# Performance work log

Measured on AMD Instinct MI355X. Metric: run time of the kernel, lower is better.

The kernel has to match this reference:

```python
import jax, jax.numpy as jnp
import numpy as np

IMAGE_SIZE = 128
FACES_PER_PIXEL = 4
BLUR_RADIUS = 0.01
EPS = 1e-8


def setup_inputs() -> dict:
    key = jax.random.key(0)
    k1, k2, k3 = jax.random.split(key, 3)
    B, V, F = 2, 2000, 800
    # verts are already projected to screen/NDC space: x,y in [-1,1], z > 0 (depth)
    xy = jax.random.uniform(k1, (B, V, 2), minval=-1.0, maxval=1.0)
    z = jax.random.uniform(k2, (B, V, 1), minval=0.5, maxval=2.5)
    verts = jnp.concatenate([xy, z], axis=-1).astype(jnp.float32)
    faces = jax.random.randint(k3, (F, 3), 0, V)
    return {"verts": verts, "faces": faces}


def _edge(a, b, p):
    # signed parallelogram area of (a -> b -> p), using xy components only
    return (p[..., 0] - a[..., 0]) * (b[..., 1] - a[..., 1]) - (
        p[..., 1] - a[..., 1]) * (b[..., 0] - a[..., 0])


def _seg_dist2(p, a, b):
    # squared distance from point p to segment [a, b] in 2D
    ab = b - a
    pa = p - a
    t = jnp.clip(jnp.sum(pa * ab, -1) / (jnp.sum(ab * ab, -1) + EPS), 0.0, 1.0)
    d = pa - t[..., None] * ab
    return jnp.sum(d * d, -1)


def _rasterize(verts, faces):
    H = W = IMAGE_SIZE
    K = FACES_PER_PIXEL
    B = verts.shape[0]
    fv = verts[:, faces]                      # [B,F,3,3] gather face vertices
    v0, v1, v2 = fv[:, :, 0], fv[:, :, 1], fv[:, :, 2]
    a0 = v0[:, None, :, :2]                   # [B,1,F,2]
    a1 = v1[:, None, :, :2]
    a2 = v2[:, None, :, :2]
    z0 = v0[:, None, :, 2]                    # [B,1,F]
    z1 = v1[:, None, :, 2]
    z2 = v2[:, None, :, 2]
    # pixel centers in NDC, pytorch3d convention: index 0 -> +1, last -> -1
    xs = 1.0 - 2.0 * (jnp.arange(W, dtype=verts.dtype) + 0.5) / W
    ys = 1.0 - 2.0 * (jnp.arange(H, dtype=verts.dtype) + 0.5) / H
    yy, xx = jnp.meshgrid(ys, xs, indexing="ij")
    p = jnp.stack([xx, yy], -1).reshape(1, -1, 1, 2)   # [1,P,1,2], P=H*W

    area = _edge(a0, a1, a2)                  # [B,1,F] signed face area*2
    w0 = _edge(a1, a2, p)                     # [B,P,F]
    w1 = _edge(a2, a0, p)
    w2 = _edge(a0, a1, p)
    denom = jnp.where(jnp.abs(area) > EPS, area,
                      jnp.where(area >= 0, EPS, -EPS))
    b0, b1, b2 = w0 / denom, w1 / denom, w2 / denom
    zpix = b0 * z0 + b1 * z1 + b2 * z2        # [B,P,F] interpolated depth

    inside = (b0 >= 0) & (b1 >= 0) & (b2 >= 0)
    dmin = jnp.minimum(_seg_dist2(p, a0, a1),
                       jnp.minimum(_seg_dist2(p, a1, a2),
                                   _seg_dist2(p, a2, a0)))
    dsign = jnp.where(inside, -dmin, dmin)    # signed squared edge distance

    valid = (inside | (dmin < BLUR_RADIUS)) & (zpix > EPS) & (
        jnp.abs(area) > EPS)
    zcand = jnp.where(valid, zpix, jnp.inf)
    _, idx = jax.lax.top_k(-zcand, K)         # K nearest faces per pixel

    take = lambda x: jnp.take_along_axis(x, idx, axis=-1)
    sel_valid = take(valid)
    pix_to_face = jnp.where(sel_valid, idx, -1)
    zbuf = jnp.where(sel_valid, take(zpix), -1.0)
    bary = jnp.stack([b0, b1, b2], -1)        # [B,P,F,3]
    bsel = jnp.take_along_axis(bary, idx[..., None], axis=2)  # [B,P,K,3]
    bsel = jnp.where(sel_valid[..., None], bsel, -1.0)
    dsel = jnp.where(sel_valid, take(dsign), -1.0)

    return (pix_to_face.reshape(B, H, W, K),
            zbuf.reshape(B, H, W, K),
            bsel.reshape(B, H, W, K, 3),
            dsel.reshape(B, H, W, K))


def reference(verts, faces):
    # Fragments: (pix_to_face, zbuf, bary_coords, dists)
    return _rasterize(verts, faces)
```

## Files before the change

### kernel.cpp

```cpp
#include <hip/hip_runtime.h>

#define IMG   128
#define KF    4
#define NF    800
#define NV    2000
#define NB    2
#define EPSF  1e-8f
#define BLURF 0.01f
#define CULL_D2 0.0103f
#define HEXT    0.0547f

typedef unsigned long long u64;
#define INVK ((((u64)0x7f800000u) << 32) | 0xffffffffu)

#pragma clang fp contract(off)

__device__ __forceinline__ float rcp2(float d) {
    float y = __builtin_amdgcn_rcpf(d);
    float e = __builtin_fmaf(-d, y, 1.0f);
    y = __builtin_fmaf(y, e, y);
    e = __builtin_fmaf(-d, y, 1.0f);
    y = __builtin_fmaf(y, e, y);
    return y;
}
__device__ __forceinline__ float fdivr(float n, float d, float y) {
    float q0 = n * y;
    float r  = __builtin_fmaf(-d, q0, n);
    return __builtin_fmaf(r, y, q0);
}

__device__ __forceinline__ float seg_d2(float pax, float pay, float abx, float aby) {
#pragma clang fp contract(off)
    float dd = (abx * abx + aby * aby) + EPSF;
    float t  = (pax * abx + pay * aby) / dd;
    t = fminf(fmaxf(t, 0.0f), 1.0f);
    float dx = pax - t * abx;
    float dy = pay - t * aby;
    return dx * dx + dy * dy;
}

__device__ __forceinline__ float seg_d2y(float pax, float pay, float abx, float aby, float y) {
#pragma clang fp contract(off)
    float dd = (abx * abx + aby * aby) + EPSF;
    float n  = pax * abx + pay * aby;
    float t  = fdivr(n, dd, y);
    t = fminf(fmaxf(t, 0.0f), 1.0f);
    float dx = pax - t * abx;
    float dy = pay - t * aby;
    return dx * dx + dy * dy;
}

__device__ __forceinline__ void ins4(u64& s0, u64& s1, u64& s2, u64& s3, u64 k) {
    bool c0 = k < s0, c1 = k < s1, c2 = k < s2, c3 = k < s3;
    s3 = c2 ? s2 : (c3 ? k : s3);
    s2 = c1 ? s1 : (c2 ? k : s2);
    s1 = c0 ? s0 : (c1 ? k : s1);
    s0 = c0 ? k  : s0;
}

__global__ __launch_bounds__(256) void raster_p1(
    const float* __restrict__ verts,
    const int*   __restrict__ faces,
    u64* __restrict__ ws,
    int sh)
{
#pragma clang fp contract(off)
    extern __shared__ __align__(16) float sFD[];
    __shared__ u64 sK[2 * 4 * 64];
    __shared__ int sTot;

    const int S     = 1 << sh;
    const int chunk = NF >> sh;

    const int tid   = threadIdx.x;
    const int blk   = blockIdx.x;
    const int tile  = blk >> sh;
    const int slice = blk & (S - 1);
    const int b     = tile >> 8;
    const int trow  = (tile & 255) >> 4;
    const int tcol  = tile & 15;
    const float* vb = verts + b * NV * 3;
    const int fbase = slice * chunk;

    if (tid == 0) sTot = 0;

    const float txmax = 1.0f - (2.0f * ((float)(tcol * 8)     + 0.5f)) / 128.0f;
    const float txmin = 1.0f - (2.0f * ((float)(tcol * 8 + 7) + 0.5f)) / 128.0f;
    const float tymax = 1.0f - (2.0f * ((float)(trow * 8)     + 0.5f)) / 128.0f;
    const float tymin = 1.0f - (2.0f * ((float)(trow * 8 + 7) + 0.5f)) / 128.0f;
    const float cx = 0.5f * (txmin + txmax);
    const float cy = 0.5f * (tymin + tymax);

    __syncthreads();

    for (int j = tid; j < chunk; j += 256) {
        int f = fbase + j;
        int i0 = faces[3 * f + 0], i1 = faces[3 * f + 1], i2 = faces[3 * f + 2];
        float a0x = vb[3 * i0], a0y = vb[3 * i0 + 1], z0 = vb[3 * i0 + 2];
        float a1x = vb[3 * i1], a1y = vb[3 * i1 + 1], z1 = vb[3 * i1 + 2];
        float a2x = vb[3 * i2], a2y = vb[3 * i2 + 1], z2 = vb[3 * i2 + 2];
        float area = (a2x - a0x) * (a1y - a0y) - (a2y - a0y) * (a1x - a0x);
        bool surv = fabsf(area) > EPSF;
        float bxmin = fminf(a0x, fminf(a1x, a2x)) - 0.101f;
        float bxmax = fmaxf(a0x, fmaxf(a1x, a2x)) + 0.101f;
        float bymin = fminf(a0y, fminf(a1y, a2y)) - 0.101f;
        float bymax = fmaxf(a0y, fmaxf(a1y, a2y)) + 0.101f;
        surv &= !(bxmin > txmax || bxmax < txmin || bymin > tymax || bymax < tymin);
        float s = (area >= 0.0f) ? 1.0f : -1.0f;
        float e0x = a2x - a1x, e0y = a2y - a1y;
        float e1x = a0x - a2x, e1y = a0y - a2y;
        float e2x = a1x - a0x, e2y = a1y - a0y;
        float w0 = s * ((cx - a1x) * e0y - (cy - a1y) * e0x) + HEXT * (fabsf(e0x) + fabsf(e0y));
        float w1 = s * ((cx - a2x) * e1y - (cy - a2y) * e1x) + HEXT * (fabsf(e1x) + fabsf(e1y));
        float w2 = s * ((cx - a0x) * e2y - (cy - a0y) * e2x) + HEXT * (fabsf(e2x) + fabsf(e2y));
        float l0 = e0x * e0x + e0y * e0y;
        float l1 = e1x * e1x + e1y * e1y;
        float l2 = e2x * e2x + e2y * e2y;
        surv &= !((w0 < 0.0f) & (w0 * w0 > CULL_D2 * l0));
        surv &= !((w1 < 0.0f) & (w1 * w1 > CULL_D2 * l1));
        surv &= !((w2 < 0.0f) & (w2 * w2 > CULL_D2 * l2));
        if (surv) {
            int pos = atomicAdd(&sTot, 1);
            float yd  = rcp2(area);
            float ylA = rcp2(l2 + EPSF);
            float ylB = rcp2(l0 + EPSF);
            float ylC = rcp2(l1 + EPSF);
            float4* fd = (float4*)&sFD[pos * 16];
            fd[0] = make_float4(a0x, a0y, a1x, a1y);
            fd[1] = make_float4(a2x, a2y, z0, z1);
            fd[2] = make_float4(z2, area, yd, __int_as_float(f));
            fd[3] = make_float4(ylA, ylB, ylC, 0.0f);
        }
    }
    __syncthreads();
    const int total = sTot;

    const int wave = tid >> 6;
    const int lane = tid & 63;
    const int pr = lane >> 3, pc = lane & 7;
    const int row = trow * 8 + pr, col = tcol * 8 + pc;
    const float px = 1.0f - (2.0f * ((float)col + 0.5f)) / 128.0f;
    const float py = 1.0f - (2.0f * ((float)row + 0.5f)) / 128.0f;

    u64 s0 = INVK, s1 = INVK, s2 = INVK, s3 = INVK;
    for (int j = wave; j < total; j += 4) {
        const float4* fd = (const float4*)&sFD[j * 16];
        float4 r0 = fd[0];
        float4 r1 = fd[1];
        float4 r2 = fd[2];
        float4 r3 = fd[3];
        float a0x = r0.x, a0y = r0.y, a1x = r0.z, a1y = r0.w;
        float a2x = r1.x, a2y = r1.y, z0 = r1.z, z1 = r1.w;
        float z2 = r2.x, denom = r2.y, yd = r2.z;
        unsigned fi = __float_as_uint(r2.w);
        float ylA = r3.x, ylB = r3.y, ylC = r3.z;

        float e0x = a2x - a1x, e0y = a2y - a1y;
        float e1x = a0x - a2x, e1y = a0y - a2y;
        float e2x = a1x - a0x, e2y = a1y - a0y;
        float p0x = px - a0x, p0y = py - a0y;
        float p1x = px - a1x, p1y = py - a1y;
        float p2x = px - a2x, p2y = py - a2y;
        float w0 = p1x * e0y - p1y * e0x;
        float w1 = p2x * e1y - p2y * e1x;
        float w2 = p0x * e2y - p0y * e2x;
        float b0 = fdivr(w0, denom, yd);
        float b1 = fdivr(w1, denom, yd);
        float b2 = fdivr(w2, denom, yd);
        float zpix = (b0 * z0 + b1 * z1) + b2 * z2;
        bool inside = fminf(b0, fminf(b1, b2)) >= 0.0f;
        bool valid;
        if (__all(inside)) {
            valid = (zpix > EPSF);
        } else {
            float dA = seg_d2y(p0x, p0y, e2x, e2y, ylA);
            float dB = seg_d2y(p1x, p1y, e0x, e0y, ylB);
            float dC = seg_d2y(p2x, p2y, e1x, e1y, ylC);
            float dmin = fminf(dA, fminf(dB, dC));
            valid = (inside | (dmin < BLURF)) & (zpix > EPSF);
        }
        u64 key = valid ? ((((u64)__float_as_uint(zpix)) << 32) | (u64)fi) : INVK;
        if (__any(key < s3)) ins4(s0, s1, s2, s3, key);
    }

    if (wave >= 2) {
        int r = wave - 2;
        sK[(r * 4 + 0) * 64 + lane] = s0;
        sK[(r * 4 + 1) * 64 + lane] = s1;
        sK[(r * 4 + 2) * 64 + lane] = s2;
        sK[(r * 4 + 3) * 64 + lane] = s3;
    }
    __syncthreads();
    if (wave < 2) {
        ins4(s0, s1, s2, s3, sK[(wave * 4 + 0) * 64 + lane]);
        ins4(s0, s1, s2, s3, sK[(wave * 4 + 1) * 64 + lane]);
        ins4(s0, s1, s2, s3, sK[(wave * 4 + 2) * 64 + lane]);
        ins4(s0, s1, s2, s3, sK[(wave * 4 + 3) * 64 + lane]);
    }
    __syncthreads();
    if (wave == 1) {
        sK[0 * 64 + lane] = s0;
        sK[1 * 64 + lane] = s1;
        sK[2 * 64 + lane] = s2;
        sK[3 * 64 + lane] = s3;
    }
    __syncthreads();
    if (wave == 0) {
        ins4(s0, s1, s2, s3, sK[0 * 64 + lane]);
        ins4(s0, s1, s2, s3, sK[1 * 64 + lane]);
        ins4(s0, s1, s2, s3, sK[2 * 64 + lane]);
        ins4(s0, s1, s2, s3, sK[3 * 64 + lane]);
        u64* wrow = ws + (size_t)blk * 256;
        wrow[0 * 64 + lane] = s0;
        wrow[1 * 64 + lane] = s1;
        wrow[2 * 64 + lane] = s2;
        wrow[3 * 64 + lane] = s3;
    }
}

__global__ __launch_bounds__(256) void raster_p2(
    const float* __restrict__ verts,
    const int*   __restrict__ faces,
    const u64* __restrict__ ws,
    int sh,
    float* __restrict__ out0, float* __restrict__ out1,
    float* __restrict__ out2, float* __restrict__ out3)
{
#pragma clang fp contract(off)
    __shared__ u64 sK[4 * 64];
    const int S    = 1 << sh;
    const int tid  = threadIdx.x;
    const int tile = blockIdx.x;
    const int b    = tile >> 8;
    const int trow = (tile & 255) >> 4;
    const int tcol = tile & 15;
    const float* vb = verts + b * NV * 3;

    if (tid < 64) {
        u64 s0 = INVK, s1 = INVK, s2 = INVK, s3 = INVK;
        const u64* base = ws + (size_t)tile * S * 256;
        for (int s = 0; s < S; ++s) {
            ins4(s0, s1, s2, s3, base[s * 256 + 0 * 64 + tid]);
            ins4(s0, s1, s2, s3, base[s * 256 + 1 * 64 + tid]);
            ins4(s0, s1, s2, s3, base[s * 256 + 2 * 64 + tid]);
            ins4(s0, s1, s2, s3, base[s * 256 + 3 * 64 + tid]);
        }
        sK[0 * 64 + tid] = s0;
        sK[1 * 64 + tid] = s1;
        sK[2 * 64 + tid] = s2;
        sK[3 * 64 + tid] = s3;
    }
    __syncthreads();

    int pix = tid >> 2, k = tid & 3;
    u64 key = sK[k * 64 + pix];
    int prow = pix >> 3, pcol = pix & 7;
    int grow = trow * 8 + prow, gcol = tcol * 8 + pcol;
    int p = (b * IMG + grow) * IMG + gcol;
    float qx = 1.0f - (2.0f * ((float)gcol + 0.5f)) / 128.0f;
    float qy = 1.0f - (2.0f * ((float)grow + 0.5f)) / 128.0f;
    float o0 = -1.0f, o1 = -1.0f, ob0 = -1.0f, ob1 = -1.0f, ob2 = -1.0f, o3 = -1.0f;
    if ((unsigned)(key >> 32) != 0x7f800000u) {
        int fi = (int)(unsigned)(key & 0xffffffffu);
        int i0 = faces[3 * fi + 0], i1 = faces[3 * fi + 1], i2 = faces[3 * fi + 2];
        float a0x = vb[3 * i0], a0y = vb[3 * i0 + 1], z0 = vb[3 * i0 + 2];
        float a1x = vb[3 * i1], a1y = vb[3 * i1 + 1], z1 = vb[3 * i1 + 2];
        float a2x = vb[3 * i2], a2y = vb[3 * i2 + 1], z2 = vb[3 * i2 + 2];
        float area = (a2x - a0x) * (a1y - a0y) - (a2y - a0y) * (a1x - a0x);
        float aab  = fabsf(area);
        float denom = (aab > EPSF) ? area : (area >= 0.0f ? EPSF : -EPSF);
        float e0x = a2x - a1x, e0y = a2y - a1y;
        float e1x = a0x - a2x, e1y = a0y - a2y;
        float e2x = a1x - a0x, e2y = a1y - a0y;
        float p0x = qx - a0x, p0y = qy - a0y;
        float p1x = qx - a1x, p1y = qy - a1y;
        float p2x = qx - a2x, p2y = qy - a2y;
        float w0 = p1x * e0y - p1y * e0x;
        float w1 = p2x * e1y - p2y * e1x;
        float w2 = p0x * e2y - p0y * e2x;
        float b0 = w0 / denom, b1 = w1 / denom, b2 = w2 / denom;
        float zpix = (b0 * z0 + b1 * z1) + b2 * z2;
        bool inside = (b0 >= 0.0f) & (b1 >= 0.0f) & (b2 >= 0.0f);
        float dA = seg_d2(p0x, p0y, e2x, e2y);
        float dB = seg_d2(p1x, p1y, e0x, e0y);
        float dC = seg_d2(p2x, p2y, e1x, e1y);
        float dmin = fminf(dA, fminf(dB, dC));
        o0 = (float)fi;
        o1 = zpix;
        ob0 = b0; ob1 = b1; ob2 = b2;
        o3 = inside ? -dmin : dmin;
    }
    int o = p * KF + k;
    out0[o] = o0;
    out1[o] = o1;
    out2[o * 3 + 0] = ob0;
    out2[o * 3 + 1] = ob1;
    out2[o * 3 + 2] = ob2;
    out3[o] = o3;
}

extern "C" void kernel_launch(void* const* d_in, const int* in_sizes, int n_in,
                              void* d_out, int out_size, void* d_ws, size_t ws_size,
                              hipStream_t stream) {
    const float* verts = (const float*)d_in[0];
    const int*   faces = (const int*)d_in[1];
    float* out = (float*)d_out;
    const int n0 = NB * IMG * IMG * KF;

    const size_t per_slice = 512ull * 256 * sizeof(u64);
    int sh;
    if      (ws_size >= 4 * per_slice) sh = 2;
    else if (ws_size >= 2 * per_slice) sh = 1;
    else                               sh = 0;
    const int S = 1 << sh;
    const int chunk = NF >> sh;
    const size_t dyn = (size_t)chunk * 16 * sizeof(float);

    raster_p1<<<dim3(512 * S), dim3(256), dyn, stream>>>(verts, faces, (u64*)d_ws, sh);
    raster_p2<<<dim3(512), dim3(256), 0, stream>>>(verts, faces, (const u64*)d_ws, sh,
        out,
        out + n0,
        out + 2 * n0,
        out + 5 * n0);
}
```

Before: 81.62 us.

## Bin surviving faces by conservative min depth and early-exit per-pixel loop

Each surviving face gets a conservative minimum depth over the tile corners and is bucketed into one of eight depth bins. Faces are compacted into shared memory in bin order using a prefix sum. The per-pixel loop walks bins front to back and stops once every lane's fourth-best key lies below the next bin's lower bound, skipping far faces. This adds an extra barrier, a serial prefix step and per-face corner depth evaluation. It depends on the slack constants and the sliver-area fallback being conservative enough to keep results exact.

```diff
diff --git a/kernel.cpp b/kernel.cpp
--- a/kernel.cpp
+++ b/kernel.cpp
@@ -9,6 +9,8 @@
 #define BLURF 0.01f
 #define CULL_D2 0.0103f
 #define HEXT    0.0547f
+#define AREA_SLIVER 0.01f
+#define ZSLACK  0.05f
 
 typedef unsigned long long u64;
 #define INVK ((((u64)0x7f800000u) << 32) | 0xffffffffu)
@@ -58,6 +60,45 @@
     s0 = c0 ? k  : s0;
 }
 
+__device__ __forceinline__ u64 eval_rec(const float4* fd, float px, float py) {
+#pragma clang fp contract(off)
+    float4 r0 = fd[0];
+    float4 r1 = fd[1];
+    float4 r2 = fd[2];
+    float4 r3 = fd[3];
+    float a0x = r0.x, a0y = r0.y, a1x = r0.z, a1y = r0.w;
+    float a2x = r1.x, a2y = r1.y, z0 = r1.z, z1 = r1.w;
+    float z2 = r2.x, denom = r2.y, yd = r2.z;
+    unsigned fi = __float_as_uint(r2.w);
+    float ylA = r3.x, ylB = r3.y, ylC = r3.z;
+
+    float e0x = a2x - a1x, e0y = a2y - a1y;
+    float e1x = a0x - a2x, e1y = a0y - a2y;
+    float e2x = a1x - a0x, e2y = a1y - a0y;
+    float p0x = px - a0x, p0y = py - a0y;
+    float p1x = px - a1x, p1y = py - a1y;
+    float p2x = px - a2x, p2y = py - a2y;
+    float w0 = p1x * e0y - p1y * e0x;
+    float w1 = p2x * e1y - p2y * e1x;
+    float w2 = p0x * e2y - p0y * e2x;
+    float b0 = fdivr(w0, denom, yd);
+    float b1 = fdivr(w1, denom, yd);
+    float b2 = fdivr(w2, denom, yd);
+    float zpix = (b0 * z0 + b1 * z1) + b2 * z2;
+    bool inside = fminf(b0, fminf(b1, b2)) >= 0.0f;
+    bool valid;
+    if (__all(inside)) {
+        valid = (zpix > EPSF);
+    } else {
+        float dA = seg_d2y(p0x, p0y, e2x, e2y, ylA);
+        float dB = seg_d2y(p1x, p1y, e0x, e0y, ylB);
+        float dC = seg_d2y(p2x, p2y, e1x, e1y, ylC);
+        float dmin = fminf(dA, fminf(dB, dC));
+        valid = (inside | (dmin < BLURF)) & (zpix > EPSF);
+    }
+    return valid ? ((((u64)__float_as_uint(zpix)) << 32) | (u64)fi) : INVK;
+}
+
 __global__ __launch_bounds__(256) void raster_p1(
     const float* __restrict__ verts,
     const int*   __restrict__ faces,
@@ -68,6 +109,9 @@
     extern __shared__ __align__(16) float sFD[];
     __shared__ u64 sK[2 * 4 * 64];
     __shared__ int sTot;
+    __shared__ int binCnt[8];
+    __shared__ int binCur[8];
+    __shared__ int binStartS[9];
 
     const int S     = 1 << sh;
     const int chunk = NF >> sh;
@@ -83,6 +127,7 @@
     const int fbase = slice * chunk;
 
     if (tid == 0) sTot = 0;
+    if (tid < 8) binCnt[tid] = 0;
 
     const float txmax = 1.0f - (2.0f * ((float)(tcol * 8)     + 0.5f)) / 128.0f;
     const float txmin = 1.0f - (2.0f * ((float)(tcol * 8 + 7) + 0.5f)) / 128.0f;
@@ -93,47 +138,126 @@
 
     __syncthreads();
 
-    for (int j = tid; j < chunk; j += 256) {
-        int f = fbase + j;
-        int i0 = faces[3 * f + 0], i1 = faces[3 * f + 1], i2 = faces[3 * f + 2];
-        float a0x = vb[3 * i0], a0y = vb[3 * i0 + 1], z0 = vb[3 * i0 + 2];
-        float a1x = vb[3 * i1], a1y = vb[3 * i1 + 1], z1 = vb[3 * i1 + 2];
-        float a2x = vb[3 * i2], a2y = vb[3 * i2 + 1], z2 = vb[3 * i2 + 2];
-        float area = (a2x - a0x) * (a1y - a0y) - (a2y - a0y) * (a1x - a0x);
-        bool surv = fabsf(area) > EPSF;
-        float bxmin = fminf(a0x, fminf(a1x, a2x)) - 0.101f;
-        float bxmax = fmaxf(a0x, fmaxf(a1x, a2x)) + 0.101f;
-        float bymin = fminf(a0y, fminf(a1y, a2y)) - 0.101f;
-        float bymax = fmaxf(a0y, fmaxf(a1y, a2y)) + 0.101f;
-        surv &= !(bxmin > txmax || bxmax < txmin || bymin > tymax || bymax < tymin);
-        float s = (area >= 0.0f) ? 1.0f : -1.0f;
-        float e0x = a2x - a1x, e0y = a2y - a1y;
-        float e1x = a0x - a2x, e1y = a0y - a2y;
-        float e2x = a1x - a0x, e2y = a1y - a0y;
-        float w0 = s * ((cx - a1x) * e0y - (cy - a1y) * e0x) + HEXT * (fabsf(e0x) + fabsf(e0y));
-        float w1 = s * ((cx - a2x) * e1y - (cy - a2y) * e1x) + HEXT * (fabsf(e1x) + fabsf(e1y));
-        float w2 = s * ((cx - a0x) * e2y - (cy - a0y) * e2x) + HEXT * (fabsf(e2x) + fabsf(e2y));
-        float l0 = e0x * e0x + e0y * e0y;
-        float l1 = e1x * e1x + e1y * e1y;
-        float l2 = e2x * e2x + e2y * e2y;
-        surv &= !((w0 < 0.0f) & (w0 * w0 > CULL_D2 * l0));
-        surv &= !((w1 < 0.0f) & (w1 * w1 > CULL_D2 * l1));
-        surv &= !((w2 < 0.0f) & (w2 * w2 > CULL_D2 * l2));
+    if (chunk <= 256) {
+        bool surv = false;
+        int bin = 0;
+        float a0x=0, a0y=0, a1x=0, a1y=0, a2x=0, a2y=0, z0=0, z1=0, z2=0;
+        float area=0, yd=0, ylA=0, ylB=0, ylC=0;
+        int f = fbase + tid;
+        if (tid < chunk) {
+            int i0 = faces[3 * f + 0], i1 = faces[3 * f + 1], i2 = faces[3 * f + 2];
+            a0x = vb[3 * i0]; a0y = vb[3 * i0 + 1]; z0 = vb[3 * i0 + 2];
+            a1x = vb[3 * i1]; a1y = vb[3 * i1 + 1]; z1 = vb[3 * i1 + 2];
+            a2x = vb[3 * i2]; a2y = vb[3 * i2 + 1]; z2 = vb[3 * i2 + 2];
+            area = (a2x - a0x) * (a1y - a0y) - (a2y - a0y) * (a1x - a0x);
+            surv = fabsf(area) > EPSF;
+            float bxmin = fminf(a0x, fminf(a1x, a2x)) - 0.101f;
+            float bxmax = fmaxf(a0x, fmaxf(a1x, a2x)) + 0.101f;
+            float bymin = fminf(a0y, fminf(a1y, a2y)) - 0.101f;
+            float bymax = fmaxf(a0y, fmaxf(a1y, a2y)) + 0.101f;
+            surv &= !(bxmin > txmax || bxmax < txmin || bymin > tymax || bymax < tymin);
+            float s = (area >= 0.0f) ? 1.0f : -1.0f;
+            float e0x = a2x - a1x, e0y = a2y - a1y;
+            float e1x = a0x - a2x, e1y = a0y - a2y;
+            float e2x = a1x - a0x, e2y = a1y - a0y;
+            float w0 = s * ((cx - a1x) * e0y - (cy - a1y) * e0x) + HEXT * (fabsf(e0x) + fabsf(e0y));
+            float w1 = s * ((cx - a2x) * e1y - (cy - a2y) * e1x) + HEXT * (fabsf(e1x) + fabsf(e1y));
+            float w2 = s * ((cx - a0x) * e2y - (cy - a0y) * e2x) + HEXT * (fabsf(e2x) + fabsf(e2y));
+            float l0 = e0x * e0x + e0y * e0y;
+            float l1 = e1x * e1x + e1y * e1y;
+            float l2 = e2x * e2x + e2y * e2y;
+            surv &= !((w0 < 0.0f) & (w0 * w0 > CULL_D2 * l0));
+            surv &= !((w1 < 0.0f) & (w1 * w1 > CULL_D2 * l1));
+            surv &= !((w2 < 0.0f) & (w2 * w2 > CULL_D2 * l2));
+            if (surv) {
+                yd  = rcp2(area);
+                ylA = rcp2(l2 + EPSF);
+                ylB = rcp2(l0 + EPSF);
+                ylC = rcp2(l1 + EPSF);
+                float zmn = 1e30f;
+                #pragma unroll
+                for (int c = 0; c < 4; ++c) {
+                    float X = (c & 1) ? txmax : txmin;
+                    float Y = (c & 2) ? tymax : tymin;
+                    float w0c = (X - a1x) * e0y - (Y - a1y) * e0x;
+                    float w1c = (X - a2x) * e1y - (Y - a2y) * e1x;
+                    float w2c = (X - a0x) * e2y - (Y - a0y) * e2x;
+                    float zc = ((w0c * z0 + w1c * z1) + w2c * z2) * yd;
+                    zmn = fminf(zmn, zc);
+                }
+                if (fabsf(area) < AREA_SLIVER) zmn = 0.0f;
+                int bi = (int)floorf((zmn - 0.5f) * 4.0f);
+                bin = bi < 0 ? 0 : (bi > 7 ? 7 : bi);
+                atomicAdd(&binCnt[bin], 1);
+            }
+        }
+        __syncthreads();
+        if (tid == 0) {
+            int run = 0;
+            for (int bb = 0; bb < 8; ++bb) {
+                binStartS[bb] = run;
+                binCur[bb]    = run;
+                run += binCnt[bb];
+            }
+            binStartS[8] = run;
+        }
+        __syncthreads();
         if (surv) {
-            int pos = atomicAdd(&sTot, 1);
-            float yd  = rcp2(area);
-            float ylA = rcp2(l2 + EPSF);
-            float ylB = rcp2(l0 + EPSF);
-            float ylC = rcp2(l1 + EPSF);
+            int pos = atomicAdd(&binCur[bin], 1);
             float4* fd = (float4*)&sFD[pos * 16];
             fd[0] = make_float4(a0x, a0y, a1x, a1y);
             fd[1] = make_float4(a2x, a2y, z0, z1);
             fd[2] = make_float4(z2, area, yd, __int_as_float(f));
             fd[3] = make_float4(ylA, ylB, ylC, 0.0f);
         }
-    }
-    __syncthreads();
-    const int total = sTot;
+        __syncthreads();
+    } else {
+        for (int j = tid; j < chunk; j += 256) {
+            int f = fbase + j;
+            int i0 = faces[3 * f + 0], i1 = faces[3 * f + 1], i2 = faces[3 * f + 2];
+            float a0x = vb[3 * i0], a0y = vb[3 * i0 + 1], z0 = vb[3 * i0 + 2];
+            float a1x = vb[3 * i1], a1y = vb[3 * i1 + 1], z1 = vb[3 * i1 + 2];
+            float a2x = vb[3 * i2], a2y = vb[3 * i2 + 1], z2 = vb[3 * i2 + 2];
+            float area = (a2x - a0x) * (a1y - a0y) - (a2y - a0y) * (a1x - a0x);
+            bool surv = fabsf(area) > EPSF;
+            float bxmin = fminf(a0x, fminf(a1x, a2x)) - 0.101f;
+            float bxmax = fmaxf(a0x, fmaxf(a1x, a2x)) + 0.101f;
+            float bymin = fminf(a0y, fminf(a1y, a2y)) - 0.101f;
+            float bymax = fmaxf(a0y, fmaxf(a1y, a2y)) + 0.101f;
+            surv &= !(bxmin > txmax || bxmax < txmin || bymin > tymax || bymax < tymin);
+            float s = (area >= 0.0f) ? 1.0f : -1.0f;
+            float e0x = a2x - a1x, e0y = a2y - a1y;
+            float e1x = a0x - a2x, e1y = a0y - a2y;
+            float e2x = a1x - a0x, e2y = a1y - a0y;
+            float w0 = s * ((cx - a1x) * e0y - (cy - a1y) * e0x) + HEXT * (fabsf(e0x) + fabsf(e0y));
+            float w1 = s * ((cx - a2x) * e1y - (cy - a2y) * e1x) + HEXT * (fabsf(e1x) + fabsf(e1y));
+            float w2 = s * ((cx - a0x) * e2y - (cy - a0y) * e2x) + HEXT * (fabsf(e2x) + fabsf(e2y));
+            float l0 = e0x * e0x + e0y * e0y;
+            float l1 = e1x * e1x + e1y * e1y;
+            float l2 = e2x * e2x + e2y * e2y;
+            surv &= !((w0 < 0.0f) & (w0 * w0 > CULL_D2 * l0));
+            surv &= !((w1 < 0.0f) & (w1 * w1 > CULL_D2 * l1));
+            surv &= !((w2 < 0.0f) & (w2 * w2 > CULL_D2 * l2));
+            if (surv) {
+                int pos = atomicAdd(&sTot, 1);
+                float yd  = rcp2(area);
+                float ylA = rcp2(l2 + EPSF);
+                float ylB = rcp2(l0 + EPSF);
+                float ylC = rcp2(l1 + EPSF);
+                float4* fd = (float4*)&sFD[pos * 16];
+                fd[0] = make_float4(a0x, a0y, a1x, a1y);
+                fd[1] = make_float4(a2x, a2y, z0, z1);
+                fd[2] = make_float4(z2, area, yd, __int_as_float(f));
+                fd[3] = make_float4(ylA, ylB, ylC, 0.0f);
+            }
+        }
+        __syncthreads();
+        if (tid == 0) {
+            binStartS[0] = 0;
+            for (int bb = 1; bb <= 8; ++bb) binStartS[bb] = sTot;
+        }
+        __syncthreads();
+    }
 
     const int wave = tid >> 6;
     const int lane = tid & 63;
@@ -143,44 +267,17 @@
     const float py = 1.0f - (2.0f * ((float)row + 0.5f)) / 128.0f;
 
     u64 s0 = INVK, s1 = INVK, s2 = INVK, s3 = INVK;
-    for (int j = wave; j < total; j += 4) {
-        const float4* fd = (const float4*)&sFD[j * 16];
-        float4 r0 = fd[0];
-        float4 r1 = fd[1];
-        float4 r2 = fd[2];
-        float4 r3 = fd[3];
-        float a0x = r0.x, a0y = r0.y, a1x = r0.z, a1y = r0.w;
-        float a2x = r1.x, a2y = r1.y, z0 = r1.z, z1 = r1.w;
-        float z2 = r2.x, denom = r2.y, yd = r2.z;
-        unsigned fi = __float_as_uint(r2.w);
-        float ylA = r3.x, ylB = r3.y, ylC = r3.z;
-
-        float e0x = a2x - a1x, e0y = a2y - a1y;
-        float e1x = a0x - a2x, e1y = a0y - a2y;
-        float e2x = a1x - a0x, e2y = a1y - a0y;
-        float p0x = px - a0x, p0y = py - a0y;
-        float p1x = px - a1x, p1y = py - a1y;
-        float p2x = px - a2x, p2y = py - a2y;
-        float w0 = p1x * e0y - p1y * e0x;
-        float w1 = p2x * e1y - p2y * e1x;
-        float w2 = p0x * e2y - p0y * e2x;
-        float b0 = fdivr(w0, denom, yd);
-        float b1 = fdivr(w1, denom, yd);
-        float b2 = fdivr(w2, denom, yd);
-        float zpix = (b0 * z0 + b1 * z1) + b2 * z2;
-        bool inside = fminf(b0, fminf(b1, b2)) >= 0.0f;
-        bool valid;
-        if (__all(inside)) {
-            valid = (zpix > EPSF);
-        } else {
-            float dA = seg_d2y(p0x, p0y, e2x, e2y, ylA);
-            float dB = seg_d2y(p1x, p1y, e0x, e0y, ylB);
-            float dC = seg_d2y(p2x, p2y, e1x, e1y, ylC);
-            float dmin = fminf(dA, fminf(dB, dC));
-            valid = (inside | (dmin < BLURF)) & (zpix > EPSF);
-        }
-        u64 key = valid ? ((((u64)__float_as_uint(zpix)) << 32) | (u64)fi) : INVK;
-        if (__any(key < s3)) ins4(s0, s1, s2, s3, key);
+    for (int bb = 0; bb < 8; ++bb) {
+        if (bb > 0) {
+            float bz = 0.5f + 0.25f * (float)bb - ZSLACK;
+            u64 bk = ((u64)__float_as_uint(bz)) << 32;
+            if (!__any(s3 > bk)) break;
+        }
+        const int jend = binStartS[bb + 1];
+        for (int j = binStartS[bb] + wave; j < jend; j += 4) {
+            u64 k = eval_rec((const float4*)&sFD[j * 16], px, py);
+            if (__any(k < s3)) ins4(s0, s1, s2, s3, k);
+        }
     }
 
     if (wave >= 2) {
```

After: 79.65 us (median of 2 runs). -2.4%, faster.
